# Performance work log

Measured on AMD Instinct MI355X. Metric: run time of the kernel, lower is better.

Reference implementation:

```python
import jax, jax.numpy as jnp
import numpy as np

EPS = 1e-8


def setup_inputs() -> dict:
    key = jax.random.key(0)
    k1, k2 = jax.random.split(key)
    a = jax.random.normal(k1, (1, 256, 128, 128), dtype=jnp.float32)
    b = jax.random.normal(k2, (1, 256, 128, 128), dtype=jnp.float32)
    return {"a": a, "b": b}


def reference(a, b):
    # a: [n, c, h, w] rendered feats; b: [n, c, h2, w2] style feats (n == 1)
    n, c, h, w = a.shape
    a_flat = a.reshape(n, c, -1)            # [n, c, hw]
    b_flat = b.reshape(n, c, -1)            # [n, c, h2w2]

    # argmin_cos_distance: channel-wise L2 normalize, cosine distance, argmin
    b_norm = jnp.sqrt((b_flat * b_flat).sum(1, keepdims=True) + EPS)
    b_n = b_flat / (b_norm + EPS)
    a_norm = jnp.sqrt((a_flat * a_flat).sum(1, keepdims=True) + EPS)
    a_n = a_flat / (a_norm + EPS)
    d_mat = 1.0 - jnp.einsum('ncp,ncq->npq', a_n, b_n)   # [n, hw, h2w2]
    z_best = jnp.argmin(d_mat, axis=2)                    # [n, hw]

    # nn_feat_replace: gather matched (unnormalized) style features
    idx = jnp.broadcast_to(z_best[:, None, :], b_flat.shape)
    target = jnp.take_along_axis(b_flat, idx, axis=2).reshape(n, c, h, w)

    # cos_loss(a, target): cosine distance over channel dim, mean over pixels
    an = jnp.sqrt((a * a).sum(1, keepdims=True))
    tn = jnp.sqrt((target * target).sum(1, keepdims=True))
    cossim = ((a / (an + EPS)) * (target / (tn + EPS))).sum(1)  # [n, h, w]
    return (1.0 - cossim).mean()
```

## Files before the change

### kernel.cpp

```cpp
#include <hip/hip_runtime.h>
#include <hip/hip_fp8.h>
#include <stdint.h>

#define EPS 1e-8f

constexpr int C  = 256;
constexpr int HW = 16384;
constexpr int BM = 128;
constexpr int NG = 2048;

typedef __attribute__((ext_vector_type(4))) float floatx4;
typedef long long llong2 __attribute__((ext_vector_type(2)));
typedef unsigned char u8;
typedef unsigned int u32;
typedef unsigned long long u64;

__device__ inline u8 f2fp8(float x) {
    __hip_fp8_e4m3 h(x);
    return h.__x;
}

__global__ __launch_bounds__(256) void prep_kernel(const float* __restrict__ a,
                                                   const float* __restrict__ b,
                                                   float* __restrict__ sumsq_a,
                                                   float* __restrict__ sumsq_b,
                                                   u8* __restrict__ aF, u8* __restrict__ bF) {
    __shared__ float red[16][65];
    __shared__ float invb_sh[64];
    const int tid = threadIdx.x;
    const int pg = tid & 15, tc = tid >> 4;
    const int p0 = blockIdx.x * 64, pb = pg * 4;

    float4 bv[16];
    float ss0 = 0.f, ss1 = 0.f, ss2 = 0.f, ss3 = 0.f;
    #pragma unroll
    for (int i = 0; i < 16; ++i) {
        bv[i] = *(const float4*)&b[(size_t)(tc * 16 + i) * HW + p0 + pb];
        ss0 += bv[i].x * bv[i].x; ss1 += bv[i].y * bv[i].y;
        ss2 += bv[i].z * bv[i].z; ss3 += bv[i].w * bv[i].w;
    }
    red[tc][pb] = ss0; red[tc][pb + 1] = ss1; red[tc][pb + 2] = ss2; red[tc][pb + 3] = ss3;
    __syncthreads();
    if (tid < 64) {
        float B = 0.f;
        #pragma unroll
        for (int j = 0; j < 16; ++j) B += red[j][tid];
        sumsq_b[p0 + tid] = B;
        invb_sh[tid] = 1.0f / (sqrtf(B + EPS) + EPS);
    }
    __syncthreads();

    #pragma unroll
    for (int j = 0; j < 4; ++j) {
        int p = p0 + pb + j;
        float inv = invb_sh[pb + j];
        int g = p >> 4;
        #pragma unroll
        for (int h = 0; h < 2; ++h) {
            int cb = tc * 2 + h;
            u64 wv = 0;
            #pragma unroll
            for (int k = 0; k < 8; ++k) {
                const float4& f = bv[h * 8 + k];
                float v = (j == 0) ? f.x : (j == 1) ? f.y : (j == 2) ? f.z : f.w;
                wv |= (u64)f2fp8(v * inv) << (8 * k);
            }
            int lane2 = (p & 15) + ((cb & 3) << 4);
            *(u64*)(bF + (((size_t)(g * 4 + (cb >> 3))) << 10) + lane2 * 16 + ((cb >> 2) & 1) * 8) = wv;
        }
    }

    float4 av[16];
    ss0 = ss1 = ss2 = ss3 = 0.f;
    #pragma unroll
    for (int i = 0; i < 16; ++i) {
        av[i] = *(const float4*)&a[(size_t)(tc * 16 + i) * HW + p0 + pb];
        ss0 += av[i].x * av[i].x; ss1 += av[i].y * av[i].y;
        ss2 += av[i].z * av[i].z; ss3 += av[i].w * av[i].w;
    }
    #pragma unroll
    for (int j = 0; j < 4; ++j) {
        int p = p0 + pb + j;
        int g = p >> 4;
        #pragma unroll
        for (int h = 0; h < 2; ++h) {
            int cb = tc * 2 + h;
            u64 wv = 0;
            #pragma unroll
            for (int k = 0; k < 8; ++k) {
                const float4& f = av[h * 8 + k];
                float v = (j == 0) ? f.x : (j == 1) ? f.y : (j == 2) ? f.z : f.w;
                wv |= (u64)f2fp8(v) << (8 * k);
            }
            int lane2 = (p & 15) + ((cb & 3) << 4);
            *(u64*)(aF + (((size_t)(g * 4 + (cb >> 3))) << 10) + lane2 * 16 + ((cb >> 2) & 1) * 8) = wv;
        }
    }
    red[tc][pb] = ss0; red[tc][pb + 1] = ss1; red[tc][pb + 2] = ss2; red[tc][pb + 3] = ss3;
    __syncthreads();
    if (tid < 64) {
        float A = 0.f;
        #pragma unroll
        for (int j = 0; j < 16; ++j) A += red[j][tid];
        sumsq_a[p0 + tid] = A;
    }
}

__global__ __launch_bounds__(256, 3) void gemm_argmax(const u8* __restrict__ aF,
                                                      const u8* __restrict__ bF,
                                                      u64* __restrict__ packed) {
    const int tid = threadIdx.x;
    const int w = tid >> 6, lane = tid & 63;
    const int q4 = lane >> 4, r15 = lane & 15;
    const int wm = w >> 1, wn = w & 1;

    const u32 bid = blockIdx.x;
    const u32 ng = bid & 7;
    const u32 mt = bid >> 3;
    const int p0 = (int)mt * BM;

    const u8* gA = aF + ((size_t)(mt * 8 + wm * 4) * 4) * 1024 + (u32)lane * 16;
    llong2 Afr[4][4];
    #pragma unroll
    for (int mi = 0; mi < 4; ++mi)
        #pragma unroll
        for (int cp = 0; cp < 4; ++cp)
            Afr[mi][cp] = *(const llong2*)(gA + (u32)(mi * 4 + cp) * 1024);

    const u8* gB = bF + ((size_t)(ng * 128 + wn * 2)) * 4096 + (u32)lane * 16;

    float bestv[4][4];
    u32   bestq[4][4];
    #pragma unroll
    for (int mi = 0; mi < 4; ++mi)
        #pragma unroll
        for (int reg = 0; reg < 4; ++reg) { bestv[mi][reg] = -3.4e38f; bestq[mi][reg] = 0; }

    const u32 qlane = ng * 2048 + wn * 32 + (u32)r15;

    llong2 Bfr[2][2];
    #pragma unroll
    for (int ni = 0; ni < 2; ++ni)
        Bfr[0][ni] = *(const llong2*)(gB + (u32)ni * 4096u);

    for (int qt = 0; qt < 32; ++qt) {
        floatx4 acc[4][2] = {};
        #pragma unroll
        for (int cp = 0; cp < 4; ++cp) {
            const int cur = cp & 1, nxt = cur ^ 1;
            u32 nqt = (cp == 3) ? (u32)(qt + 1 < 32 ? qt + 1 : 31) : (u32)qt;
            u32 ncp = (cp == 3) ? 0u : (u32)(cp + 1);
            #pragma unroll
            for (int ni = 0; ni < 2; ++ni)
                Bfr[nxt][ni] = *(const llong2*)(gB + nqt * 16384u + (u32)ni * 4096u + ncp * 1024u);
            #pragma unroll
            for (int mi = 0; mi < 4; ++mi)
                #pragma unroll
                for (int ni = 0; ni < 2; ++ni)
                    acc[mi][ni] = __builtin_amdgcn_mfma_f32_16x16x32_fp8_fp8(
                        Afr[mi][cp].x, Bfr[cur][ni].x, acc[mi][ni], 0, 0, 0);
            #pragma unroll
            for (int mi = 0; mi < 4; ++mi)
                #pragma unroll
                for (int ni = 0; ni < 2; ++ni)
                    acc[mi][ni] = __builtin_amdgcn_mfma_f32_16x16x32_fp8_fp8(
                        Afr[mi][cp].y, Bfr[cur][ni].y, acc[mi][ni], 0, 0, 0);
        }
        #pragma unroll
        for (int mi = 0; mi < 4; ++mi)
            #pragma unroll
            for (int ni = 0; ni < 2; ++ni) {
                u32 qc = qlane + (u32)qt * 64 + (u32)ni * 16;
                #pragma unroll
                for (int reg = 0; reg < 4; ++reg) {
                    float v = acc[mi][ni][reg];
                    bool gt = v > bestv[mi][reg];
                    bestv[mi][reg] = gt ? v : bestv[mi][reg];
                    bestq[mi][reg] = gt ? qc : bestq[mi][reg];
                }
            }
    }

    #pragma unroll
    for (int mi = 0; mi < 4; ++mi)
        #pragma unroll
        for (int reg = 0; reg < 4; ++reg) {
            u32 m = __float_as_uint(bestv[mi][reg]);
            m = m ^ (u32)(((int)m >> 31) | 0x80000000u);
            u64 pk = ((u64)m << 32) | (u64)(0xFFFFFFFFu - bestq[mi][reg]);
            #pragma unroll
            for (int d = 1; d < 16; d <<= 1) {
                u64 o = __shfl_xor((unsigned long long)pk, d);
                pk = o > pk ? o : pk;
            }
            if (r15 == 0)
                atomicMax(&packed[p0 + wm * 64 + mi * 16 + q4 * 4 + reg], pk);
        }
}

__global__ void loss_kernel(const u64* __restrict__ packed,
                            const float* __restrict__ sumsq_a, const float* __restrict__ sumsq_b,
                            float* __restrict__ out) {
    int p = blockIdx.x * 256 + threadIdx.x;
    u64 pk = packed[p];
    u32 m = (u32)(pk >> 32);
    u32 u = (m & 0x80000000u) ? (m ^ 0x80000000u) : ~m;
    float s = __uint_as_float(u);
    u32 q = 0xFFFFFFFFu - (u32)(pk & 0xFFFFFFFFull);
    float A = sumsq_a[p], B = sumsq_b[q];
    float dot = s * (sqrtf(B + EPS) + EPS);
    float cossim = dot / ((sqrtf(A) + EPS) * (sqrtf(B) + EPS));
    float v = (1.0f - cossim) * (1.0f / (float)HW);
    #pragma unroll
    for (int d = 1; d < 64; d <<= 1) v += __shfl_xor(v, d);
    if ((threadIdx.x & 63) == 0) atomicAdd(out, v);
}

extern "C" void kernel_launch(void* const* d_in, const int* in_sizes, int n_in,
                              void* d_out, int out_size, void* d_ws, size_t ws_size,
                              hipStream_t stream) {
    const float* a = (const float*)d_in[0];
    const float* b = (const float*)d_in[1];
    float* out = (float*)d_out;
    char* ws = (char*)d_ws;

    u8*    aF      = (u8*)ws;
    u8*    bF      = (u8*)(ws + (size_t)4 * 1024 * 1024);
    float* sumsq_a = (float*)(ws + (size_t)8 * 1024 * 1024);
    float* sumsq_b = sumsq_a + HW;
    u64*   packed  = (u64*)(sumsq_b + HW);

    hipMemsetAsync(out, 0, sizeof(float), stream);
    hipMemsetAsync(packed, 0, (size_t)HW * sizeof(u64), stream);

    prep_kernel<<<dim3(HW / 64), 256, 0, stream>>>(a, b, sumsq_a, sumsq_b, aF, bF);
    gemm_argmax<<<dim3((HW / BM) * (HW / NG)), 256, 0, stream>>>(aF, bF, packed);
    loss_kernel<<<dim3(HW / 256), 256, 0, stream>>>(packed, sumsq_a, sumsq_b, out);
}
```

Before: 166.5 us.

## Split style range into 16 groups and use packed fp8 conversion in prep

Halves the per-block slice of style pixels (NG 2048→1024), so the grid doubles to 16 groups per row tile and each block runs 16 instead of 32 q-tiles. This raises parallelism and shortens each block at the cost of loading the A fragments twice as often and writing twice as many partial argmax candidates for the final reduction. Separately, the prep kernel converts four floats to fp8 at once with the packed cvt_pk_fp8_f32 builtin instead of converting one byte at a time, cutting conversion and shift/or instructions.

```diff
diff --git a/kernel.cpp b/kernel.cpp
--- a/kernel.cpp
+++ b/kernel.cpp
@@ -7,7 +7,7 @@
 constexpr int C  = 256;
 constexpr int HW = 16384;
 constexpr int BM = 128;
-constexpr int NG = 2048;
+constexpr int NG = 1024;
 
 typedef __attribute__((ext_vector_type(4))) float floatx4;
 typedef long long llong2 __attribute__((ext_vector_type(2)));
@@ -18,6 +18,17 @@
 __device__ inline u8 f2fp8(float x) {
     __hip_fp8_e4m3 h(x);
     return h.__x;
+}
+
+__device__ inline u32 pk4(float va, float vb, float vc, float vd) {
+#if __has_builtin(__builtin_amdgcn_cvt_pk_fp8_f32)
+    u32 w = __builtin_amdgcn_cvt_pk_fp8_f32(va, vb, 0, false);
+    w = __builtin_amdgcn_cvt_pk_fp8_f32(vc, vd, w, true);
+    return w;
+#else
+    return (u32)f2fp8(va) | ((u32)f2fp8(vb) << 8) |
+           ((u32)f2fp8(vc) << 16) | ((u32)f2fp8(vd) << 24);
+#endif
 }
 
 __global__ __launch_bounds__(256) void prep_kernel(const float* __restrict__ a,
@@ -58,13 +69,15 @@
         #pragma unroll
         for (int h = 0; h < 2; ++h) {
             int cb = tc * 2 + h;
-            u64 wv = 0;
-            #pragma unroll
-            for (int k = 0; k < 8; ++k) {
-                const float4& f = bv[h * 8 + k];
-                float v = (j == 0) ? f.x : (j == 1) ? f.y : (j == 2) ? f.z : f.w;
-                wv |= (u64)f2fp8(v * inv) << (8 * k);
-            }
+            float s0 = ((j == 0) ? bv[h*8+0].x : (j == 1) ? bv[h*8+0].y : (j == 2) ? bv[h*8+0].z : bv[h*8+0].w) * inv;
+            float s1 = ((j == 0) ? bv[h*8+1].x : (j == 1) ? bv[h*8+1].y : (j == 2) ? bv[h*8+1].z : bv[h*8+1].w) * inv;
+            float s2 = ((j == 0) ? bv[h*8+2].x : (j == 1) ? bv[h*8+2].y : (j == 2) ? bv[h*8+2].z : bv[h*8+2].w) * inv;
+            float s3 = ((j == 0) ? bv[h*8+3].x : (j == 1) ? bv[h*8+3].y : (j == 2) ? bv[h*8+3].z : bv[h*8+3].w) * inv;
+            float s4 = ((j == 0) ? bv[h*8+4].x : (j == 1) ? bv[h*8+4].y : (j == 2) ? bv[h*8+4].z : bv[h*8+4].w) * inv;
+            float s5 = ((j == 0) ? bv[h*8+5].x : (j == 1) ? bv[h*8+5].y : (j == 2) ? bv[h*8+5].z : bv[h*8+5].w) * inv;
+            float s6 = ((j == 0) ? bv[h*8+6].x : (j == 1) ? bv[h*8+6].y : (j == 2) ? bv[h*8+6].z : bv[h*8+6].w) * inv;
+            float s7 = ((j == 0) ? bv[h*8+7].x : (j == 1) ? bv[h*8+7].y : (j == 2) ? bv[h*8+7].z : bv[h*8+7].w) * inv;
+            u64 wv = (u64)pk4(s0, s1, s2, s3) | ((u64)pk4(s4, s5, s6, s7) << 32);
             int lane2 = (p & 15) + ((cb & 3) << 4);
             *(u64*)(bF + (((size_t)(g * 4 + (cb >> 3))) << 10) + lane2 * 16 + ((cb >> 2) & 1) * 8) = wv;
         }
@@ -85,13 +98,15 @@
         #pragma unroll
         for (int h = 0; h < 2; ++h) {
             int cb = tc * 2 + h;
-            u64 wv = 0;
-            #pragma unroll
-            for (int k = 0; k < 8; ++k) {
-                const float4& f = av[h * 8 + k];
-                float v = (j == 0) ? f.x : (j == 1) ? f.y : (j == 2) ? f.z : f.w;
-                wv |= (u64)f2fp8(v) << (8 * k);
-            }
+            float s0 = (j == 0) ? av[h*8+0].x : (j == 1) ? av[h*8+0].y : (j == 2) ? av[h*8+0].z : av[h*8+0].w;
+            float s1 = (j == 0) ? av[h*8+1].x : (j == 1) ? av[h*8+1].y : (j == 2) ? av[h*8+1].z : av[h*8+1].w;
+            float s2 = (j == 0) ? av[h*8+2].x : (j == 1) ? av[h*8+2].y : (j == 2) ? av[h*8+2].z : av[h*8+2].w;
+            float s3 = (j == 0) ? av[h*8+3].x : (j == 1) ? av[h*8+3].y : (j == 2) ? av[h*8+3].z : av[h*8+3].w;
+            float s4 = (j == 0) ? av[h*8+4].x : (j == 1) ? av[h*8+4].y : (j == 2) ? av[h*8+4].z : av[h*8+4].w;
+            float s5 = (j == 0) ? av[h*8+5].x : (j == 1) ? av[h*8+5].y : (j == 2) ? av[h*8+5].z : av[h*8+5].w;
+            float s6 = (j == 0) ? av[h*8+6].x : (j == 1) ? av[h*8+6].y : (j == 2) ? av[h*8+6].z : av[h*8+6].w;
+            float s7 = (j == 0) ? av[h*8+7].x : (j == 1) ? av[h*8+7].y : (j == 2) ? av[h*8+7].z : av[h*8+7].w;
+            u64 wv = (u64)pk4(s0, s1, s2, s3) | ((u64)pk4(s4, s5, s6, s7) << 32);
             int lane2 = (p & 15) + ((cb & 3) << 4);
             *(u64*)(aF + (((size_t)(g * 4 + (cb >> 3))) << 10) + lane2 * 16 + ((cb >> 2) & 1) * 8) = wv;
         }
@@ -115,8 +130,8 @@
     const int wm = w >> 1, wn = w & 1;
 
     const u32 bid = blockIdx.x;
-    const u32 ng = bid & 7;
-    const u32 mt = bid >> 3;
+    const u32 ng = bid & 15;
+    const u32 mt = bid >> 4;
     const int p0 = (int)mt * BM;
 
     const u8* gA = aF + ((size_t)(mt * 8 + wm * 4) * 4) * 1024 + (u32)lane * 16;
@@ -127,7 +142,7 @@
         for (int cp = 0; cp < 4; ++cp)
             Afr[mi][cp] = *(const llong2*)(gA + (u32)(mi * 4 + cp) * 1024);
 
-    const u8* gB = bF + ((size_t)(ng * 128 + wn * 2)) * 4096 + (u32)lane * 16;
+    const u8* gB = bF + ((size_t)(ng * 64 + wn * 2)) * 4096 + (u32)lane * 16;
 
     float bestv[4][4];
     u32   bestq[4][4];
@@ -136,19 +151,19 @@
         #pragma unroll
         for (int reg = 0; reg < 4; ++reg) { bestv[mi][reg] = -3.4e38f; bestq[mi][reg] = 0; }
 
-    const u32 qlane = ng * 2048 + wn * 32 + (u32)r15;
+    const u32 qlane = ng * 1024 + wn * 32 + (u32)r15;
 
     llong2 Bfr[2][2];
     #pragma unroll
     for (int ni = 0; ni < 2; ++ni)
         Bfr[0][ni] = *(const llong2*)(gB + (u32)ni * 4096u);
 
-    for (int qt = 0; qt < 32; ++qt) {
+    for (int qt = 0; qt < 16; ++qt) {
         floatx4 acc[4][2] = {};
         #pragma unroll
         for (int cp = 0; cp < 4; ++cp) {
             const int cur = cp & 1, nxt = cur ^ 1;
-            u32 nqt = (cp == 3) ? (u32)(qt + 1 < 32 ? qt + 1 : 31) : (u32)qt;
+            u32 nqt = (cp == 3) ? (u32)(qt + 1 < 16 ? qt + 1 : 15) : (u32)qt;
             u32 ncp = (cp == 3) ? 0u : (u32)(cp + 1);
             #pragma unroll
             for (int ni = 0; ni < 2; ++ni)
```

After: 169.3 us. About the same (+1.7%).
